# Performance work log

Measured on AMD Instinct MI355X. Metric: run time of the kernel, lower is better.

## Reference

```python
import jax, jax.numpy as jnp
import numpy as np

HID, HEADS, FF, DEPTH = 1152, 16, 4304, 2
HD = HID // HEADS            # 72
ROT = HD // 2                # 36 (rotary_pos_emb width)
S, NSEG = 2048, 4
EPS = 1e-6


def _layernorm(x, w, b):
    m = jnp.mean(x, axis=-1, keepdims=True)
    xc = x - m
    v = jnp.mean(xc * xc, axis=-1, keepdims=True)
    return xc * jax.lax.rsqrt(v + EPS) * w + b


def _rotate_half(x):
    x1, x2 = jnp.split(x, 2, axis=-1)
    return jnp.concatenate([-x2, x1], axis=-1)


def _apply_rotary(t, freqs):
    # t: [S, H, D], freqs: [S, D/2]
    emb = jnp.concatenate([freqs, freqs], axis=-1)          # [S, D]
    cos = jnp.cos(emb)[:, None, :]
    sin = jnp.sin(emb)[:, None, :]
    return t * cos + _rotate_half(t) * sin


def setup_inputs() -> dict:
    key = jax.random.key(0)
    ks = jax.random.split(key, 16)
    sd = 0.02
    # rotary freqs as in VisionRotaryEmbedding(dim=HD//2): h-pos and w-pos halves
    inv_freq = 1.0 / (10000.0 ** (jnp.arange(0, ROT, 2, dtype=jnp.float32) / ROT))  # [18]
    pos = jnp.arange(S, dtype=jnp.float32)
    hpos, wpos = pos // 32.0, pos % 32.0
    rotary = jnp.concatenate([jnp.outer(hpos, inv_freq), jnp.outer(wpos, inv_freq)], axis=-1)  # [S, 36]
    return {
        "x": jax.random.normal(ks[0], (S, HID), jnp.float32),
        "cu_seqlens": jnp.arange(NSEG + 1, dtype=jnp.int32) * (S // NSEG),
        "rotary_pos_emb": rotary,
        "norm1_w": jnp.ones((DEPTH, HID), jnp.float32),
        "norm1_b": jnp.zeros((DEPTH, HID), jnp.float32),
        "qkv_w": jax.random.normal(ks[1], (DEPTH, 3 * HID, HID), jnp.float32) * sd,
        "qkv_b": jnp.zeros((DEPTH, 3 * HID), jnp.float32),
        "proj_w": jax.random.normal(ks[2], (DEPTH, HID, HID), jnp.float32) * sd,
        "proj_b": jnp.zeros((DEPTH, HID), jnp.float32),
        "norm2_w": jnp.ones((DEPTH, HID), jnp.float32),
        "norm2_b": jnp.zeros((DEPTH, HID), jnp.float32),
        "fc1_w": jax.random.normal(ks[3], (DEPTH, FF, HID), jnp.float32) * sd,
        "fc1_b": jnp.zeros((DEPTH, FF), jnp.float32),
        "fc2_w": jax.random.normal(ks[4], (DEPTH, HID, FF), jnp.float32) * sd,
        "fc2_b": jnp.zeros((DEPTH, HID), jnp.float32),
    }


def _forward(x, cu_seqlens, rotary_pos_emb, norm1_w, norm1_b, qkv_w, qkv_b,
             proj_w, proj_b, norm2_w, norm2_b, fc1_w, fc1_b, fc2_w, fc2_b):
    seq_len = x.shape[0]
    # block-diagonal additive mask from cu_seqlens (same mask the torch loop builds)
    seg = jnp.searchsorted(cu_seqlens, jnp.arange(seq_len, dtype=cu_seqlens.dtype), side="right") - 1
    same = seg[:, None] == seg[None, :]
    bias = jnp.where(same, jnp.float32(0.0), jnp.finfo(jnp.float32).min)  # [S, S]
    scale = 1.0 / np.sqrt(HD)
    for d in range(DEPTH):
        # --- attention ---
        h = _layernorm(x, norm1_w[d], norm1_b[d])
        qkv = (h @ qkv_w[d].T + qkv_b[d]).reshape(seq_len, 3, HEADS, HD)
        q, k, v = qkv[:, 0], qkv[:, 1], qkv[:, 2]           # [S, H, D]
        q = _apply_rotary(q, rotary_pos_emb)
        k = _apply_rotary(k, rotary_pos_emb)
        scores = jnp.einsum("qhd,khd->hqk", q, k) * scale + bias[None]
        probs = jax.nn.softmax(scores.astype(jnp.float32), axis=-1).astype(q.dtype)
        attn = jnp.einsum("hqk,khd->qhd", probs, v).reshape(seq_len, HID)
        x = x + attn @ proj_w[d].T + proj_b[d]
        # --- MLP (gelu tanh approx) ---
        h2 = _layernorm(x, norm2_w[d], norm2_b[d])
        x = x + jax.nn.gelu(h2 @ fc1_w[d].T + fc1_b[d], approximate=True) @ fc2_w[d].T + fc2_b[d]
    return x


def reference(x, cu_seqlens, rotary_pos_emb, norm1_w, norm1_b, qkv_w, qkv_b,
              proj_w, proj_b, norm2_w, norm2_b, fc1_w, fc1_b, fc2_w, fc2_b):
    return _forward(x, cu_seqlens, rotary_pos_emb, norm1_w, norm1_b, qkv_w, qkv_b,
                    proj_w, proj_b, norm2_w, norm2_b, fc1_w, fc1_b, fc2_w, fc2_b)
```

## Files before the change

kernel.cpp:

```cpp
#include <hip/hip_runtime.h>

#define S_LEN 2048
#define HID   1152
#define HEADS 16
#define HD    72
#define ROT   36
#define LD3   3456
#define FF    4304
#define FFP   4320

typedef short s16x8 __attribute__((ext_vector_type(8)));
typedef short s16x4 __attribute__((ext_vector_type(4)));
typedef float f32x4 __attribute__((ext_vector_type(4)));
typedef short bf_t;

__device__ __forceinline__ short f2b(float f) {
  unsigned u = __float_as_uint(f);
  u += 0x7fffu + ((u >> 16) & 1u);
  return (short)(u >> 16);
}
__device__ __forceinline__ float b2f(short h) {
  return __uint_as_float(((unsigned)(unsigned short)h) << 16);
}
__device__ __forceinline__ float gelu_f(float x) {
  float t = tanhf(0.7978845608028654f * (x + 0.044715f * x * x * x));
  return 0.5f * x * (1.0f + t);
}

typedef const __attribute__((address_space(1))) void* gas_p;
typedef __attribute__((address_space(3))) void* las_p;
__device__ __forceinline__ void gload16(const void* g, void* l) {
  __builtin_amdgcn_global_load_lds((gas_p)g, (las_p)l, 16, 0, 0);
}

#define QKV_OFF 0
#define P_OFF   (3456 * 1152)
#define F1_OFF  (P_OFF + 1152 * 1152)
#define F2_OFF  (F1_OFF + 4352 * 1152)
#define ARENA_ELEMS (F2_OFF + 1152 * 4320)
#define GA_Q  (8960 * 288)
#define TOT_Q (GA_Q + 1152 * 1080)

__global__ __launch_bounds__(256) void convw_all(
    const float* __restrict__ qkvw, const float* __restrict__ projw,
    const float* __restrict__ fc1w, const float* __restrict__ fc2w,
    bf_t* __restrict__ arena)
{
  int idx = blockIdx.x * 256 + threadIdx.x;
  if (idx >= TOT_Q) return;
  if (idx < GA_Q) {
    int row = idx / 288, kq = (idx % 288) * 4;
    const float* s = nullptr; bf_t* d;
    if (row < 3456)      { s = qkvw + (size_t)row * 1152;  d = arena + (size_t)row * 1152; }
    else if (row < 4608) { int r = row - 3456; s = projw + (size_t)r * 1152; d = arena + P_OFF + (size_t)r * 1152; }
    else                 { int r = row - 4608; d = arena + F1_OFF + (size_t)r * 1152;
                           if (r < FF) s = fc1w + (size_t)r * 1152; }
    s16x4 o;
    if (s) { float4 v = *(const float4*)(s + kq);
             o[0] = f2b(v.x); o[1] = f2b(v.y); o[2] = f2b(v.z); o[3] = f2b(v.w); }
    else   { o[0] = 0; o[1] = 0; o[2] = 0; o[3] = 0; }
    *(s16x4*)(d + kq) = o;
  } else {
    int q = idx - GA_Q;
    int r = q / 1080, kq = (q % 1080) * 4;
    s16x4 o;
    if (kq < FF) {
      float4 v = *(const float4*)(fc2w + (size_t)r * FF + kq);
      o[0] = f2b(v.x); o[1] = f2b(v.y); o[2] = f2b(v.z); o[3] = f2b(v.w);
    } else { o[0] = 0; o[1] = 0; o[2] = 0; o[3] = 0; }
    *(s16x4*)(arena + F2_OFF + (size_t)r * FFP + kq) = o;
  }
}

__global__ __launch_bounds__(256) void costab_kernel(
    const float* __restrict__ rot, float* __restrict__ ct, float* __restrict__ st)
{
  int i = blockIdx.x * 256 + threadIdx.x;
  if (i < S_LEN * ROT) { float f = rot[i]; ct[i] = cosf(f); st[i] = sinf(f); }
}

__global__ __launch_bounds__(256) void ln_kernel(
    const float* __restrict__ x, const float* __restrict__ wgt,
    const float* __restrict__ bia, bf_t* __restrict__ outb)
{
  const int row = blockIdx.x, tid = threadIdx.x;
  const float4* xr = (const float4*)(x + (size_t)row * HID);
  float4 a = xr[tid];
  float4 b2 = make_float4(0.f, 0.f, 0.f, 0.f);
  const bool has2 = tid < 32;
  if (has2) b2 = xr[256 + tid];
  float s = a.x + a.y + a.z + a.w + b2.x + b2.y + b2.z + b2.w;
  float q = a.x*a.x + a.y*a.y + a.z*a.z + a.w*a.w
          + b2.x*b2.x + b2.y*b2.y + b2.z*b2.z + b2.w*b2.w;
  for (int mk = 32; mk; mk >>= 1) { s += __shfl_xor(s, mk); q += __shfl_xor(q, mk); }
  __shared__ float red[16];
  if ((tid & 63) == 0) { red[tid >> 6] = s; red[8 + (tid >> 6)] = q; }
  __syncthreads();
  if (tid == 0) {
    red[4]  = red[0] + red[1] + red[2] + red[3];
    red[12] = red[8] + red[9] + red[10] + red[11];
  }
  __syncthreads();
  float mean = red[4] * (1.0f / HID);
  float var  = red[12] * (1.0f / HID) - mean * mean;
  float rstd = rsqrtf(var + 1e-6f);
  const float4* w4 = (const float4*)wgt;
  const float4* b4 = (const float4*)bia;
  s16x4* o4 = (s16x4*)(outb + (size_t)row * HID);
  {
    float4 wv = w4[tid], bv = b4[tid];
    s16x4 o;
    o[0] = f2b((a.x - mean) * rstd * wv.x + bv.x);
    o[1] = f2b((a.y - mean) * rstd * wv.y + bv.y);
    o[2] = f2b((a.z - mean) * rstd * wv.z + bv.z);
    o[3] = f2b((a.w - mean) * rstd * wv.w + bv.w);
    o4[tid] = o;
  }
  if (has2) {
    float4 wv = w4[256 + tid], bv = b4[256 + tid];
    s16x4 o;
    o[0] = f2b((b2.x - mean) * rstd * wv.x + bv.x);
    o[1] = f2b((b2.y - mean) * rstd * wv.y + bv.y);
    o[2] = f2b((b2.z - mean) * rstd * wv.z + bv.z);
    o[3] = f2b((b2.w - mean) * rstd * wv.w + bv.w);
    o4[256 + tid] = o;
  }
}

__global__ __launch_bounds__(256) void redln_kernel(
    const float* __restrict__ part, const float* __restrict__ bias,
    const float* __restrict__ resid, float* __restrict__ xout,
    bf_t* __restrict__ hout, const float* __restrict__ lnw,
    const float* __restrict__ lnb, int do_ln)
{
  const int row = blockIdx.x, tid = threadIdx.x;
  const size_t base = (size_t)row * 288;
  const float4* r4 = (const float4*)resid;
  const float4* b4 = (const float4*)bias;
  const float4* p4 = (const float4*)part;
  const bool has2 = tid < 32;

  float4 a, c;
  {
    float4 r = r4[base + tid], bv = b4[tid];
    a = make_float4(r.x + bv.x, r.y + bv.y, r.z + bv.z, r.w + bv.w);
#pragma unroll
    for (int p = 0; p < 4; p++) {
      float4 v = p4[(size_t)p * S_LEN * 288 + base + tid];
      a.x += v.x; a.y += v.y; a.z += v.z; a.w += v.w;
    }
  }
  c = make_float4(0.f, 0.f, 0.f, 0.f);
  if (has2) {
    float4 r = r4[base + 256 + tid], bv = b4[256 + tid];
    c = make_float4(r.x + bv.x, r.y + bv.y, r.z + bv.z, r.w + bv.w);
#pragma unroll
    for (int p = 0; p < 4; p++) {
      float4 v = p4[(size_t)p * S_LEN * 288 + base + 256 + tid];
      c.x += v.x; c.y += v.y; c.z += v.z; c.w += v.w;
    }
  }
  ((float4*)xout)[base + tid] = a;
  if (has2) ((float4*)xout)[base + 256 + tid] = c;

  if (!do_ln) return;

  float s = a.x + a.y + a.z + a.w + c.x + c.y + c.z + c.w;
  float q = a.x*a.x + a.y*a.y + a.z*a.z + a.w*a.w
          + c.x*c.x + c.y*c.y + c.z*c.z + c.w*c.w;
  for (int mk = 32; mk; mk >>= 1) { s += __shfl_xor(s, mk); q += __shfl_xor(q, mk); }
  __shared__ float red[16];
  if ((tid & 63) == 0) { red[tid >> 6] = s; red[8 + (tid >> 6)] = q; }
  __syncthreads();
  if (tid == 0) {
    red[4]  = red[0] + red[1] + red[2] + red[3];
    red[12] = red[8] + red[9] + red[10] + red[11];
  }
  __syncthreads();
  float mean = red[4] * (1.0f / HID);
  float var  = red[12] * (1.0f / HID) - mean * mean;
  float rstd = rsqrtf(var + 1e-6f);
  const float4* w4 = (const float4*)lnw;
  const float4* lb4 = (const float4*)lnb;
  s16x4* o4 = (s16x4*)(hout + (size_t)row * HID);
  {
    float4 wv = w4[tid], bv = lb4[tid];
    s16x4 o;
    o[0] = f2b((a.x - mean) * rstd * wv.x + bv.x);
    o[1] = f2b((a.y - mean) * rstd * wv.y + bv.y);
    o[2] = f2b((a.z - mean) * rstd * wv.z + bv.z);
    o[3] = f2b((a.w - mean) * rstd * wv.w + bv.w);
    o4[tid] = o;
  }
  if (has2) {
    float4 wv = w4[256 + tid], bv = lb4[256 + tid];
    s16x4 o;
    o[0] = f2b((c.x - mean) * rstd * wv.x + bv.x);
    o[1] = f2b((c.y - mean) * rstd * wv.y + bv.y);
    o[2] = f2b((c.z - mean) * rstd * wv.z + bv.z);
    o[3] = f2b((c.w - mean) * rstd * wv.w + bv.w);
    o4[256 + tid] = o;
  }
}

__global__ __launch_bounds__(256) void rotary_kernel(
    bf_t* __restrict__ qkv, const float* __restrict__ ct, const float* __restrict__ st)
{
  int idx = blockIdx.x * 256 + threadIdx.x;
  if (idx >= S_LEN * HEADS * ROT) return;
  int t = idx / (HEADS * ROT);
  int r = idx % (HEADS * ROT);
  int h = r / ROT, dd = r % ROT;
  float c = ct[t * ROT + dd], s = st[t * ROT + dd];
  size_t base = (size_t)t * LD3 + h * HD + dd;
  float q1 = b2f(qkv[base]),        q2 = b2f(qkv[base + ROT]);
  float k1 = b2f(qkv[base + HID]),  k2 = b2f(qkv[base + HID + ROT]);
  const float scale = 0.11785113019775793f;
  qkv[base]             = f2b((q1 * c - q2 * s) * scale);
  qkv[base + ROT]       = f2b((q2 * c + q1 * s) * scale);
  qkv[base + HID]       = f2b(k1 * c - k2 * s);
  qkv[base + HID + ROT] = f2b(k2 * c + k1 * s);
}

template<int MODE>
__global__ __launch_bounds__(256, 4) void gemm1(
    const bf_t* __restrict__ A, int lda,
    const bf_t* __restrict__ B, int ldb,
    const float* __restrict__ bias, int nbias,
    void* outp, int ldc, int nvalid, int K, int kchunk)
{
  __shared__ __align__(16) bf_t As[128 * 32];
  __shared__ __align__(16) bf_t Bs[128 * 32];
  const int tid = threadIdx.x;
  const int l = tid & 63, w = tid >> 6;
  const int lr = l & 15, lg = l >> 4;
  const int wm = (w >> 1) * 64, wn = (w & 1) * 64;

  unsigned gx = gridDim.x, gy = gridDim.y, gz = gridDim.z;
  unsigned nwg = gx * gy * gz;
  unsigned lin = (blockIdx.z * gy + blockIdx.y) * gx + blockIdx.x;
  if ((nwg & 7u) == 0u) {
    unsigned q = nwg >> 3;
    lin = (lin & 7u) * q + (lin >> 3);
  }
  const unsigned bz = lin / (gx * gy);
  const unsigned rem = lin % (gx * gy);
  const unsigned by = rem / gx, bx = rem % gx;

  const int rowA0 = by * 128, colB0 = bx * 128;
  const int kb0 = bz * kchunk;
  int kb1 = kb0 + kchunk; if (kb1 > K) kb1 = K;

  const int o1 = tid * 16, o2 = o1 + 4096;
  const int r1 = o1 >> 6, c1 = o1 & 63;
  const int r2 = o2 >> 6, c2 = o2 & 63;
  const char* Ab = (const char*)A;
  const char* Bb = (const char*)B;

  f32x4 acc[4][4] = {};

  for (int kb = kb0; kb < kb1; kb += 32) {
    gload16(Ab + ((size_t)(rowA0 + r1) * lda + kb) * 2 + c1, (char*)As + o1);
    gload16(Ab + ((size_t)(rowA0 + r2) * lda + kb) * 2 + c2, (char*)As + o2);
    gload16(Bb + ((size_t)(colB0 + r1) * ldb + kb) * 2 + c1, (char*)Bs + o1);
    gload16(Bb + ((size_t)(colB0 + r2) * ldb + kb) * 2 + c2, (char*)Bs + o2);
    asm volatile("s_waitcnt vmcnt(0)" ::: "memory");
    __syncthreads();
    s16x8 af[4], bv[4];
#pragma unroll
    for (int mt = 0; mt < 4; mt++) af[mt] = *(const s16x8*)&As[(wm + mt * 16 + lr) * 32 + lg * 8];
#pragma unroll
    for (int nt = 0; nt < 4; nt++) bv[nt] = *(const s16x8*)&Bs[(wn + nt * 16 + lr) * 32 + lg * 8];
#pragma unroll
    for (int mt = 0; mt < 4; mt++)
#pragma unroll
      for (int nt = 0; nt < 4; nt++)
        acc[mt][nt] = __builtin_amdgcn_mfma_f32_16x16x32_bf16(af[mt], bv[nt], acc[mt][nt], 0, 0, 0);
    __syncthreads();
  }

#pragma unroll
  for (int mt = 0; mt < 4; mt++) {
    const int rr = rowA0 + wm + mt * 16 + lg * 4;
#pragma unroll
    for (int nt = 0; nt < 4; nt++) {
      const int cc = colB0 + wn + nt * 16 + lr;
#pragma unroll
      for (int i = 0; i < 4; i++) {
        const int row = rr + i;
        float* P = (float*)outp + (size_t)bz * ((size_t)S_LEN * ldc);
        P[(size_t)row * ldc + cc] = acc[mt][nt][i];
      }
    }
  }
}

template<int MODE>
__global__ __launch_bounds__(256, 4) void gemm2(
    const bf_t* __restrict__ A, int lda,
    const bf_t* __restrict__ B, int ldb,
    const float* __restrict__ bias, int nbias,
    void* outp, int ldc, int nvalid, int K, int kchunk)
{
  __shared__ __align__(16) bf_t As[2][128 * 32];
  __shared__ __align__(16) bf_t Bs[2][64 * 32];
  const int tid = threadIdx.x;
  const int l = tid & 63, w = tid >> 6;
  const int lr = l & 15, lg = l >> 4;
  const int wm = (w >> 1) * 64, wn = (w & 1) * 32;

  unsigned gx = gridDim.x, gy = gridDim.y, gz = gridDim.z;
  unsigned nwg = gx * gy * gz;
  unsigned lin = (blockIdx.z * gy + blockIdx.y) * gx + blockIdx.x;
  if ((nwg & 7u) == 0u) {
    unsigned q = nwg >> 3;
    lin = (lin & 7u) * q + (lin >> 3);
  }
  const unsigned bz = lin / (gx * gy);
  const unsigned rem = lin % (gx * gy);
  const unsigned by = rem / gx, bx = rem % gx;

  const int rowA0 = by * 128, colB0 = bx * 64;
  const int kb0 = bz * kchunk;
  int kb1 = kb0 + kchunk; if (kb1 > K) kb1 = K;

  const int oA1 = tid * 16, oA2 = oA1 + 4096;
  const int rA1 = oA1 >> 6, cA1 = oA1 & 63;
  const int rA2 = rA1 + 64;
  const int oB = tid * 16;
  const int rB = oB >> 6, cB = oB & 63;
  const char* Ab = (const char*)A;
  const char* Bb = (const char*)B;

#define STAGE(buf, kk) do { \
    gload16(Ab + ((size_t)(rowA0 + rA1) * lda + (kk)) * 2 + cA1, (char*)As[buf] + oA1); \
    gload16(Ab + ((size_t)(rowA0 + rA2) * lda + (kk)) * 2 + cA1, (char*)As[buf] + oA2); \
    gload16(Bb + ((size_t)(colB0 + rB)  * ldb + (kk)) * 2 + cB,  (char*)Bs[buf] + oB);  \
  } while (0)

  f32x4 acc[4][2] = {};

  STAGE(0, kb0);
  asm volatile("s_waitcnt vmcnt(0)" ::: "memory");
  __builtin_amdgcn_s_barrier();
  __builtin_amdgcn_sched_barrier(0);

  int cur = 0;
  for (int kb = kb0; kb < kb1; kb += 32) {
    if (kb + 32 < kb1) STAGE(cur ^ 1, kb + 32);
    s16x8 af[4], bv[2];
#pragma unroll
    for (int mt = 0; mt < 4; mt++)
      af[mt] = *(const s16x8*)&As[cur][(wm + mt * 16 + lr) * 32 + lg * 8];
#pragma unroll
    for (int nt = 0; nt < 2; nt++)
      bv[nt] = *(const s16x8*)&Bs[cur][(wn + nt * 16 + lr) * 32 + lg * 8];
    asm volatile("s_waitcnt lgkmcnt(0)" ::: "memory");
    __builtin_amdgcn_sched_barrier(0);
#pragma unroll
    for (int mt = 0; mt < 4; mt++)
#pragma unroll
      for (int nt = 0; nt < 2; nt++)
        acc[mt][nt] = __builtin_amdgcn_mfma_f32_16x16x32_bf16(af[mt], bv[nt], acc[mt][nt], 0, 0, 0);
    asm volatile("s_waitcnt vmcnt(0)" ::: "memory");
    __builtin_amdgcn_s_barrier();
    __builtin_amdgcn_sched_barrier(0);
    cur ^= 1;
  }
#undef STAGE

#pragma unroll
  for (int mt = 0; mt < 4; mt++) {
    const int rr = rowA0 + wm + mt * 16 + lg * 4;
#pragma unroll
    for (int nt = 0; nt < 2; nt++) {
      const int cc = colB0 + wn + nt * 16 + lr;
      const float bvl = (cc < nbias) ? bias[cc] : 0.0f;
#pragma unroll
      for (int i = 0; i < 4; i++) {
        float v = acc[mt][nt][i] + bvl;
        const int row = rr + i;
        if (MODE == 0) {
          ((bf_t*)outp)[(size_t)row * ldc + cc] = f2b(v);
        } else if (MODE == 2) {
          if (cc < nvalid)      ((bf_t*)outp)[(size_t)row * ldc + cc] = f2b(gelu_f(v));
          else if (cc < ldc)    ((bf_t*)outp)[(size_t)row * ldc + cc] = 0;
        } else {
          float* P = (float*)outp + (size_t)bz * ((size_t)S_LEN * ldc);
          P[(size_t)row * ldc + cc] = v;
        }
      }
    }
  }
}

#define QSTR 104
#define VSTR 76
#define PSTR 72
__global__ __launch_bounds__(512, 2) void attn_kernel(
    const bf_t* __restrict__ qkv, const int* __restrict__ cu, int nseg,
    bf_t* __restrict__ outb)
{
  __shared__ __align__(16) bf_t Qs[128 * QSTR];
  __shared__ __align__(16) bf_t Ks[2][64 * QSTR];
  __shared__ __align__(16) bf_t VTs[2][80 * VSTR];
  __shared__ __align__(16) bf_t Pb[8][16 * PSTR];
  const int tid = threadIdx.x;
  const int l = tid & 63, w = tid >> 6;
  const int lr = l & 15, lg = l >> 4;
  const int h = blockIdx.y;
  const int qbase = blockIdx.x * 128;

  int kstart = 0, kend = S_LEN;
  for (int s2 = 0; s2 < nseg; s2++) {
    int a = cu[s2], b = cu[s2 + 1];
    if (qbase >= a && qbase < b) { kstart = a; kend = b; }
  }

  for (int i = tid; i < 128 * QSTR; i += 512)
    if ((i % QSTR) >= HD) Qs[i] = 0;
  for (int i = tid; i < 64 * QSTR; i += 512)
    if ((i % QSTR) >= HD) { Ks[0][i] = 0; Ks[1][i] = 0; }
  for (int i = tid; i < 80 * VSTR; i += 512)
    if ((i / VSTR) >= HD) { VTs[0][i] = 0; VTs[1][i] = 0; }
  for (int c = tid; c < 1152; c += 512) {
    int r = c / 9, j = c % 9;
    *(s16x8*)&Qs[r * QSTR + j * 8] =
        *(const s16x8*)&qkv[(size_t)(qbase + r) * LD3 + h * HD + j * 8];
  }
  {
#pragma unroll
    for (int u = 0; u < 2; u++) {
      int c = tid + u * 512;
      if (c < 576) {
        int r = c / 9, j = c % 9;
        int gr = kstart + r; if (gr >= kend) gr = kend - 1;
        *(s16x8*)&Ks[0][r * QSTR + j * 8] =
            *(const s16x8*)&qkv[(size_t)gr * LD3 + HID + h * HD + j * 8];
      }
    }
#pragma unroll
    for (int u = 0; u < 2; u++) {
      int c = tid + u * 512;
      if (c < 576) {
        int r = c & 63, j = c >> 6;
        int gr = kstart + r; if (gr >= kend) gr = kend - 1;
        s16x8 v = *(const s16x8*)&qkv[(size_t)gr * LD3 + 2 * HID + h * HD + j * 8];
#pragma unroll
        for (int jj = 0; jj < 8; jj++) VTs[0][(j * 8 + jj) * VSTR + r] = v[jj];
      }
    }
  }
  __syncthreads();

  s16x8 qf[3];
#pragma unroll
  for (int ks = 0; ks < 3; ks++)
    qf[ks] = *(const s16x8*)&Qs[(w * 16 + lr) * QSTR + ks * 32 + lg * 8];

  float m_i[4], l_i[4];
  f32x4 Of[5] = {};
#pragma unroll
  for (int i = 0; i < 4; i++) { m_i[i] = -1e30f; l_i[i] = 0.0f; }

  const int ntile = (kend - kstart + 63) >> 6;
  int cur = 0;
  for (int t = 0; t < ntile; t++) {
    const int kb = kstart + t * 64;
    const bool more = (t + 1 < ntile);

    s16x8 kreg[2], vreg[2];
    if (more) {
      const int nb = kb + 64;
#pragma unroll
      for (int u = 0; u < 2; u++) {
        int c = tid + u * 512;
        if (c < 576) {
          int r = c / 9, j = c % 9;
          int gr = nb + r; if (gr >= kend) gr = kend - 1;
          kreg[u] = *(const s16x8*)&qkv[(size_t)gr * LD3 + HID + h * HD + j * 8];
        }
      }
#pragma unroll
      for (int u = 0; u < 2; u++) {
        int c = tid + u * 512;
        if (c < 576) {
          int r = c & 63, j = c >> 6;
          int gr = nb + r; if (gr >= kend) gr = kend - 1;
          vreg[u] = *(const s16x8*)&qkv[(size_t)gr * LD3 + 2 * HID + h * HD + j * 8];
        }
      }
    }

    f32x4 sc[4] = {};
#pragma unroll
    for (int kc = 0; kc < 4; kc++) {
#pragma unroll
      for (int ks = 0; ks < 3; ks++) {
        s16x8 kf = *(const s16x8*)&Ks[cur][(kc * 16 + lr) * QSTR + ks * 32 + lg * 8];
        sc[kc] = __builtin_amdgcn_mfma_f32_16x16x32_bf16(qf[ks], kf, sc[kc], 0, 0, 0);
      }
    }
#pragma unroll
    for (int kc = 0; kc < 4; kc++) {
      if ((kb + kc * 16 + lr) >= kend) {
#pragma unroll
        for (int i = 0; i < 4; i++) sc[kc][i] = -1e30f;
      }
    }
    float tmax[4], scl[4], rs[4];
#pragma unroll
    for (int i = 0; i < 4; i++) {
      float tm = fmaxf(fmaxf(sc[0][i], sc[1][i]), fmaxf(sc[2][i], sc[3][i]));
#pragma unroll
      for (int d2 = 1; d2 < 16; d2 <<= 1) tm = fmaxf(tm, __shfl_xor(tm, d2));
      tmax[i] = tm;
    }
#pragma unroll
    for (int i = 0; i < 4; i++) {
      float mn = fmaxf(m_i[i], tmax[i]);
      scl[i] = __expf(m_i[i] - mn);
      m_i[i] = mn;
      rs[i] = 0.0f;
    }
#pragma unroll
    for (int kc = 0; kc < 4; kc++)
#pragma unroll
      for (int i = 0; i < 4; i++) {
        float p = __expf(sc[kc][i] - m_i[i]);
        sc[kc][i] = p;
        rs[i] += p;
      }
#pragma unroll
    for (int i = 0; i < 4; i++) {
#pragma unroll
      for (int d2 = 1; d2 < 16; d2 <<= 1) rs[i] += __shfl_xor(rs[i], d2);
      l_i[i] = l_i[i] * scl[i] + rs[i];
    }
#pragma unroll
    for (int nt = 0; nt < 5; nt++)
#pragma unroll
      for (int i = 0; i < 4; i++) Of[nt][i] *= scl[i];
#pragma unroll
    for (int kc = 0; kc < 4; kc++)
#pragma unroll
      for (int i = 0; i < 4; i++)
        Pb[w][(lg * 4 + i) * PSTR + kc * 16 + lr] = f2b(sc[kc][i]);
    asm volatile("s_waitcnt lgkmcnt(0)" ::: "memory");
    __builtin_amdgcn_sched_barrier(0);
    s16x8 pf[2];
#pragma unroll
    for (int k2 = 0; k2 < 2; k2++)
      pf[k2] = *(const s16x8*)&Pb[w][lr * PSTR + k2 * 32 + lg * 8];
#pragma unroll
    for (int nt = 0; nt < 5; nt++) {
#pragma unroll
      for (int k2 = 0; k2 < 2; k2++) {
        const int vb = (nt * 16 + lr) * VSTR + k2 * 32 + lg * 8;
        s16x4 va = *(const s16x4*)&VTs[cur][vb];
        s16x4 vb2 = *(const s16x4*)&VTs[cur][vb + 4];
        s16x8 vf;
        vf[0] = va[0]; vf[1] = va[1]; vf[2] = va[2]; vf[3] = va[3];
        vf[4] = vb2[0]; vf[5] = vb2[1]; vf[6] = vb2[2]; vf[7] = vb2[3];
        Of[nt] = __builtin_amdgcn_mfma_f32_16x16x32_bf16(pf[k2], vf, Of[nt], 0, 0, 0);
      }
    }

    if (more) {
#pragma unroll
      for (int u = 0; u < 2; u++) {
        int c = tid + u * 512;
        if (c < 576) {
          int r = c / 9, j = c % 9;
          *(s16x8*)&Ks[cur ^ 1][r * QSTR + j * 8] = kreg[u];
        }
      }
#pragma unroll
      for (int u = 0; u < 2; u++) {
        int c = tid + u * 512;
        if (c < 576) {
          int r = c & 63, j = c >> 6;
#pragma unroll
          for (int jj = 0; jj < 8; jj++)
            VTs[cur ^ 1][(j * 8 + jj) * VSTR + r] = vreg[u][jj];
        }
      }
    }
    __syncthreads();
    cur ^= 1;
  }

  float inv[4];
#pragma unroll
  for (int i = 0; i < 4; i++) inv[i] = 1.0f / l_i[i];
#pragma unroll
  for (int nt = 0; nt < 5; nt++) {
    int cc = nt * 16 + lr;
    if (cc < HD) {
#pragma unroll
      for (int i = 0; i < 4; i++) {
        int row = qbase + w * 16 + lg * 4 + i;
        outb[(size_t)row * HID + h * HD + cc] = f2b(Of[nt][i] * inv[i]);
      }
    }
  }
}

extern "C" void kernel_launch(void* const* d_in, const int* in_sizes, int n_in,
                              void* d_out, int out_size, void* d_ws, size_t ws_size,
                              hipStream_t stream) {
  const float* x     = (const float*)d_in[0];
  const int*   cu    = (const int*)d_in[1];
  const float* rotab = (const float*)d_in[2];
  const float* n1w   = (const float*)d_in[3];
  const float* n1b   = (const float*)d_in[4];
  const float* qkvw  = (const float*)d_in[5];
  const float* qkvb  = (const float*)d_in[6];
  const float* projw = (const float*)d_in[7];
  const float* projb = (const float*)d_in[8];
  const float* n2w   = (const float*)d_in[9];
  const float* n2b   = (const float*)d_in[10];
  const float* fc1w  = (const float*)d_in[11];
  const float* fc1b  = (const float*)d_in[12];
  const float* fc2w  = (const float*)d_in[13];
  const float* fc2b  = (const float*)d_in[14];
  float* out = (float*)d_out;
  char* ws = (char*)d_ws;

  size_t off = 0;
  float* xbuf = (float*)(ws + off); off += (size_t)S_LEN * HID * 4;
  bf_t* hbf   = (bf_t*)(ws + off);  off += (size_t)S_LEN * HID * 2;
  bf_t* qkvbf = (bf_t*)(ws + off);
  bf_t* ff1bf = (bf_t*)(ws + off);  off += (size_t)S_LEN * FFP * 2;
  bf_t* attnbf= (bf_t*)(ws + off);  off += (size_t)S_LEN * HID * 2;
  bf_t* arena = (bf_t*)(ws + off);  off += (size_t)ARENA_ELEMS * 2;
  float* ctab = (float*)(ws + off); off += (size_t)S_LEN * ROT * 4;
  float* stab = (float*)(ws + off); off += (size_t)S_LEN * ROT * 4;
  float* part = (float*)(ws + off); off += (size_t)4 * S_LEN * HID * 4;

  costab_kernel<<<(S_LEN * ROT + 255) / 256, 256, 0, stream>>>(rotab, ctab, stab);

  const int nseg = in_sizes[1] - 1;

  for (int d = 0; d < 2; d++) {
    const float* xin = (d == 0) ? x : xbuf;
    convw_all<<<(TOT_Q + 255) / 256, 256, 0, stream>>>(
        qkvw + (size_t)d * LD3 * HID, projw + (size_t)d * HID * HID,
        fc1w + (size_t)d * FF * HID, fc2w + (size_t)d * HID * FF, arena);
    if (d == 0)
      ln_kernel<<<S_LEN, 256, 0, stream>>>(x, n1w, n1b, hbf);
    gemm2<0><<<dim3(LD3 / 64, 16), 256, 0, stream>>>(
        hbf, HID, arena + QKV_OFF, HID, qkvb + (size_t)d * LD3, LD3,
        qkvbf, LD3, LD3, HID, HID);
    rotary_kernel<<<(S_LEN * HEADS * ROT + 255) / 256, 256, 0, stream>>>(qkvbf, ctab, stab);
    attn_kernel<<<dim3(S_LEN / 128, HEADS), 512, 0, stream>>>(qkvbf, cu, nseg, attnbf);
    gemm1<3><<<dim3(HID / 128, 16, 4), 256, 0, stream>>>(
        attnbf, HID, arena + P_OFF, HID, nullptr, 0, part, HID, HID, HID, 288);
    redln_kernel<<<S_LEN, 256, 0, stream>>>(
        part, projb + (size_t)d * HID, xin, xbuf, hbf,
        n2w + (size_t)d * HID, n2b + (size_t)d * HID, 1);
    gemm2<2><<<dim3((FFP + 63) / 64, 16), 256, 0, stream>>>(
        hbf, HID, arena + F1_OFF, HID, fc1b + (size_t)d * FF, FF,
        ff1bf, FFP, FF, HID, HID);
    gemm1<3><<<dim3(HID / 128, 16, 4), 256, 0, stream>>>(
        ff1bf, FFP, arena + F2_OFF, FFP, nullptr, 0, part, HID, HID, FFP, 1088);
    if (d == 0) {
      redln_kernel<<<S_LEN, 256, 0, stream>>>(
          part, fc2b, xbuf, xbuf, hbf, n1w + HID, n1b + HID, 1);
    } else {
      redln_kernel<<<S_LEN, 256, 0, stream>>>(
          part, fc2b + (size_t)HID, xbuf, out, nullptr, nullptr, nullptr, 0);
    }
  }
}
```

Before: 402.0 us.

## Replace LDS-staged GEMMs with direct global-to-register MFMA operand loads

Both GEMM kernels are merged into one kernel that loads the MFMA operand fragments straight from global memory into registers, with no LDS staging, barriers or double buffering. The split-K projection and fc2 GEMMs move from 128x128 tiles to 128x64 tiles, which doubles their grid. This removes LDS traffic and synchronisation but gives up the cross-wave reuse that shared memory provided, so each wave fetches its own operands and relies on L1/L2 caching. The strided 16-byte row loads may be less coalesced than the previous staged copies.

```diff
diff --git a/kernel.cpp b/kernel.cpp
--- a/kernel.cpp
+++ b/kernel.cpp
@@ -25,12 +25,6 @@
 __device__ __forceinline__ float gelu_f(float x) {
   float t = tanhf(0.7978845608028654f * (x + 0.044715f * x * x * x));
   return 0.5f * x * (1.0f + t);
-}
-
-typedef const __attribute__((address_space(1))) void* gas_p;
-typedef __attribute__((address_space(3))) void* las_p;
-__device__ __forceinline__ void gload16(const void* g, void* l) {
-  __builtin_amdgcn_global_load_lds((gas_p)g, (las_p)l, 16, 0, 0);
 }
 
 #define QKV_OFF 0
@@ -223,18 +217,16 @@
 }
 
 template<int MODE>
-__global__ __launch_bounds__(256, 4) void gemm1(
+__global__ __launch_bounds__(256, 4) void gemm_direct(
     const bf_t* __restrict__ A, int lda,
     const bf_t* __restrict__ B, int ldb,
     const float* __restrict__ bias, int nbias,
     void* outp, int ldc, int nvalid, int K, int kchunk)
 {
-  __shared__ __align__(16) bf_t As[128 * 32];
-  __shared__ __align__(16) bf_t Bs[128 * 32];
   const int tid = threadIdx.x;
   const int l = tid & 63, w = tid >> 6;
   const int lr = l & 15, lg = l >> 4;
-  const int wm = (w >> 1) * 64, wn = (w & 1) * 64;
+  const int wm = (w >> 1) * 64, wn = (w & 1) * 32;
 
   unsigned gx = gridDim.x, gy = gridDim.y, gz = gridDim.z;
   unsigned nwg = gx * gy * gz;
@@ -247,127 +239,33 @@
   const unsigned rem = lin % (gx * gy);
   const unsigned by = rem / gx, bx = rem % gx;
 
-  const int rowA0 = by * 128, colB0 = bx * 128;
-  const int kb0 = bz * kchunk;
-  int kb1 = kb0 + kchunk; if (kb1 > K) kb1 = K;
-
-  const int o1 = tid * 16, o2 = o1 + 4096;
-  const int r1 = o1 >> 6, c1 = o1 & 63;
-  const int r2 = o2 >> 6, c2 = o2 & 63;
-  const char* Ab = (const char*)A;
-  const char* Bb = (const char*)B;
-
-  f32x4 acc[4][4] = {};
-
-  for (int kb = kb0; kb < kb1; kb += 32) {
-    gload16(Ab + ((size_t)(rowA0 + r1) * lda + kb) * 2 + c1, (char*)As + o1);
-    gload16(Ab + ((size_t)(rowA0 + r2) * lda + kb) * 2 + c2, (char*)As + o2);
-    gload16(Bb + ((size_t)(colB0 + r1) * ldb + kb) * 2 + c1, (char*)Bs + o1);
-    gload16(Bb + ((size_t)(colB0 + r2) * ldb + kb) * 2 + c2, (char*)Bs + o2);
-    asm volatile("s_waitcnt vmcnt(0)" ::: "memory");
-    __syncthreads();
-    s16x8 af[4], bv[4];
-#pragma unroll
-    for (int mt = 0; mt < 4; mt++) af[mt] = *(const s16x8*)&As[(wm + mt * 16 + lr) * 32 + lg * 8];
-#pragma unroll
-    for (int nt = 0; nt < 4; nt++) bv[nt] = *(const s16x8*)&Bs[(wn + nt * 16 + lr) * 32 + lg * 8];
-#pragma unroll
-    for (int mt = 0; mt < 4; mt++)
-#pragma unroll
-      for (int nt = 0; nt < 4; nt++)
-        acc[mt][nt] = __builtin_amdgcn_mfma_f32_16x16x32_bf16(af[mt], bv[nt], acc[mt][nt], 0, 0, 0);
-    __syncthreads();
-  }
-
-#pragma unroll
-  for (int mt = 0; mt < 4; mt++) {
-    const int rr = rowA0 + wm + mt * 16 + lg * 4;
-#pragma unroll
-    for (int nt = 0; nt < 4; nt++) {
-      const int cc = colB0 + wn + nt * 16 + lr;
-#pragma unroll
-      for (int i = 0; i < 4; i++) {
-        const int row = rr + i;
-        float* P = (float*)outp + (size_t)bz * ((size_t)S_LEN * ldc);
-        P[(size_t)row * ldc + cc] = acc[mt][nt][i];
-      }
-    }
-  }
-}
-
-template<int MODE>
-__global__ __launch_bounds__(256, 4) void gemm2(
-    const bf_t* __restrict__ A, int lda,
-    const bf_t* __restrict__ B, int ldb,
-    const float* __restrict__ bias, int nbias,
-    void* outp, int ldc, int nvalid, int K, int kchunk)
-{
-  __shared__ __align__(16) bf_t As[2][128 * 32];
-  __shared__ __align__(16) bf_t Bs[2][64 * 32];
-  const int tid = threadIdx.x;
-  const int l = tid & 63, w = tid >> 6;
-  const int lr = l & 15, lg = l >> 4;
-  const int wm = (w >> 1) * 64, wn = (w & 1) * 32;
-
-  unsigned gx = gridDim.x, gy = gridDim.y, gz = gridDim.z;
-  unsigned nwg = gx * gy * gz;
-  unsigned lin = (blockIdx.z * gy + blockIdx.y) * gx + blockIdx.x;
-  if ((nwg & 7u) == 0u) {
-    unsigned q = nwg >> 3;
-    lin = (lin & 7u) * q + (lin >> 3);
-  }
-  const unsigned bz = lin / (gx * gy);
-  const unsigned rem = lin % (gx * gy);
-  const unsigned by = rem / gx, bx = rem % gx;
-
   const int rowA0 = by * 128, colB0 = bx * 64;
   const int kb0 = bz * kchunk;
   int kb1 = kb0 + kchunk; if (kb1 > K) kb1 = K;
 
-  const int oA1 = tid * 16, oA2 = oA1 + 4096;
-  const int rA1 = oA1 >> 6, cA1 = oA1 & 63;
-  const int rA2 = rA1 + 64;
-  const int oB = tid * 16;
-  const int rB = oB >> 6, cB = oB & 63;
-  const char* Ab = (const char*)A;
-  const char* Bb = (const char*)B;
-
-#define STAGE(buf, kk) do { \
-    gload16(Ab + ((size_t)(rowA0 + rA1) * lda + (kk)) * 2 + cA1, (char*)As[buf] + oA1); \
-    gload16(Ab + ((size_t)(rowA0 + rA2) * lda + (kk)) * 2 + cA1, (char*)As[buf] + oA2); \
-    gload16(Bb + ((size_t)(colB0 + rB)  * ldb + (kk)) * 2 + cB,  (char*)Bs[buf] + oB);  \
-  } while (0)
+  const bf_t* ap[4];
+  const bf_t* bp[2];
+#pragma unroll
+  for (int mt = 0; mt < 4; mt++)
+    ap[mt] = A + (size_t)(rowA0 + wm + mt * 16 + lr) * lda + kb0 + lg * 8;
+#pragma unroll
+  for (int nt = 0; nt < 2; nt++)
+    bp[nt] = B + (size_t)(colB0 + wn + nt * 16 + lr) * ldb + kb0 + lg * 8;
 
   f32x4 acc[4][2] = {};
 
-  STAGE(0, kb0);
-  asm volatile("s_waitcnt vmcnt(0)" ::: "memory");
-  __builtin_amdgcn_s_barrier();
-  __builtin_amdgcn_sched_barrier(0);
-
-  int cur = 0;
   for (int kb = kb0; kb < kb1; kb += 32) {
-    if (kb + 32 < kb1) STAGE(cur ^ 1, kb + 32);
     s16x8 af[4], bv[2];
 #pragma unroll
-    for (int mt = 0; mt < 4; mt++)
-      af[mt] = *(const s16x8*)&As[cur][(wm + mt * 16 + lr) * 32 + lg * 8];
-#pragma unroll
-    for (int nt = 0; nt < 2; nt++)
-      bv[nt] = *(const s16x8*)&Bs[cur][(wn + nt * 16 + lr) * 32 + lg * 8];
-    asm volatile("s_waitcnt lgkmcnt(0)" ::: "memory");
-    __builtin_amdgcn_sched_barrier(0);
+    for (int mt = 0; mt < 4; mt++) { af[mt] = *(const s16x8*)ap[mt]; ap[mt] += 32; }
+#pragma unroll
+    for (int nt = 0; nt < 2; nt++) { bv[nt] = *(const s16x8*)bp[nt]; bp[nt] += 32; }
 #pragma unroll
     for (int mt = 0; mt < 4; mt++)
 #pragma unroll
       for (int nt = 0; nt < 2; nt++)
         acc[mt][nt] = __builtin_amdgcn_mfma_f32_16x16x32_bf16(af[mt], bv[nt], acc[mt][nt], 0, 0, 0);
-    asm volatile("s_waitcnt vmcnt(0)" ::: "memory");
-    __builtin_amdgcn_s_barrier();
-    __builtin_amdgcn_sched_barrier(0);
-    cur ^= 1;
-  }
-#undef STAGE
+  }
 
 #pragma unroll
   for (int mt = 0; mt < 4; mt++) {
@@ -375,7 +273,8 @@
 #pragma unroll
     for (int nt = 0; nt < 2; nt++) {
       const int cc = colB0 + wn + nt * 16 + lr;
-      const float bvl = (cc < nbias) ? bias[cc] : 0.0f;
+      if (MODE == 2 && cc >= ldc) continue;
+      const float bvl = (MODE == 3) ? 0.0f : ((cc < nbias) ? bias[cc] : 0.0f);
 #pragma unroll
       for (int i = 0; i < 4; i++) {
         float v = acc[mt][nt][i] + bvl;
@@ -384,7 +283,7 @@
           ((bf_t*)outp)[(size_t)row * ldc + cc] = f2b(v);
         } else if (MODE == 2) {
           if (cc < nvalid)      ((bf_t*)outp)[(size_t)row * ldc + cc] = f2b(gelu_f(v));
-          else if (cc < ldc)    ((bf_t*)outp)[(size_t)row * ldc + cc] = 0;
+          else                  ((bf_t*)outp)[(size_t)row * ldc + cc] = 0;
         } else {
           float* P = (float*)outp + (size_t)bz * ((size_t)S_LEN * ldc);
           P[(size_t)row * ldc + cc] = v;
@@ -649,20 +548,20 @@
         fc1w + (size_t)d * FF * HID, fc2w + (size_t)d * HID * FF, arena);
     if (d == 0)
       ln_kernel<<<S_LEN, 256, 0, stream>>>(x, n1w, n1b, hbf);
-    gemm2<0><<<dim3(LD3 / 64, 16), 256, 0, stream>>>(
+    gemm_direct<0><<<dim3(LD3 / 64, 16), 256, 0, stream>>>(
         hbf, HID, arena + QKV_OFF, HID, qkvb + (size_t)d * LD3, LD3,
         qkvbf, LD3, LD3, HID, HID);
     rotary_kernel<<<(S_LEN * HEADS * ROT + 255) / 256, 256, 0, stream>>>(qkvbf, ctab, stab);
     attn_kernel<<<dim3(S_LEN / 128, HEADS), 512, 0, stream>>>(qkvbf, cu, nseg, attnbf);
-    gemm1<3><<<dim3(HID / 128, 16, 4), 256, 0, stream>>>(
+    gemm_direct<3><<<dim3(HID / 64, 16, 4), 256, 0, stream>>>(
         attnbf, HID, arena + P_OFF, HID, nullptr, 0, part, HID, HID, HID, 288);
     redln_kernel<<<S_LEN, 256, 0, stream>>>(
         part, projb + (size_t)d * HID, xin, xbuf, hbf,
         n2w + (size_t)d * HID, n2b + (size_t)d * HID, 1);
-    gemm2<2><<<dim3((FFP + 63) / 64, 16), 256, 0, stream>>>(
+    gemm_direct<2><<<dim3((FFP + 63) / 64, 16), 256, 0, stream>>>(
         hbf, HID, arena + F1_OFF, HID, fc1b + (size_t)d * FF, FF,
         ff1bf, FFP, FF, HID, HID);
-    gemm1<3><<<dim3(HID / 128, 16, 4), 256, 0, stream>>>(
+    gemm_direct<3><<<dim3(HID / 64, 16, 4), 256, 0, stream>>>(
         ff1bf, FFP, arena + F2_OFF, FFP, nullptr, 0, part, HID, HID, FFP, 1088);
     if (d == 0) {
       redln_kernel<<<S_LEN, 256, 0, stream>>>(
```

New measurement: 856.7 us. +113.1%, slower.
